# Kernel tuning notes

Measured on AMD Instinct MI355X. Metric: run time of the kernel, lower is better.

The kernel has to match this reference:

```python
import jax, jax.numpy as jnp
import numpy as np


def rosa_batch(bits):
    """Vectorized ROSA (suffix-automaton 'predict next symbol of longest previously
    seen suffix') for a batch of binary sequences.

    bits: [N, T] int32 in {0,1}. Returns [N, T] int32 in {-1, 0, 1}.

    Equivalent to the serial suffix-automaton: at step i, let L = max_{j<i}
    lcs(i, j) (longest common suffix of prefixes ending at i and j). If L == 0
    the answer is -1; otherwise let e = max{ j < i : lcs(i, j) == L } (most
    recent occurrence end, matching the automaton's last-endpos bookkeeping)
    and the answer is bits[e + 1]. lcs follows the standard recurrence
    lcs(i, j) = (x[i] == x[j]) * (lcs(i-1, j-1) + 1), computed with a scan
    over i carrying the length-T lcs row, vmapped implicitly over N.
    """
    N, T = bits.shape
    jpos = jnp.arange(T)

    def step(prev, it):
        i, xt = it  # i: scalar step index, xt: [N] current symbols
        # prev[:, j] = lcs(i-1, j); shift to get lcs(i-1, j-1)
        shifted = jnp.concatenate([jnp.zeros((N, 1), prev.dtype), prev[:, :-1]], axis=1)
        cur = jnp.where(bits == xt[:, None], shifted + 1, 0)  # [N, T] lcs(i, j)
        valid = jpos[None, :] < i
        cm = jnp.where(valid, cur, -1)
        L = cm.max(axis=1)  # [N] longest previously-seen suffix length
        # most recent j < i achieving the max
        e = jnp.where(valid & (cm == L[:, None]), jpos[None, :], -1).max(axis=1)
        nxt = jnp.take_along_axis(bits, jnp.clip(e + 1, 0, T - 1)[:, None], axis=1)[:, 0]
        y = jnp.where(L > 0, nxt, -1)
        return cur, y

    _, ys = jax.lax.scan(step, jnp.zeros((N, T), jnp.int32), (jnp.arange(T), bits.T))
    return ys.T


def rosa_bits_btc(bits_btc):
    """bits_btc: [B, T, C] -> idx [B, T, C]; ROSA runs along T per (b, c)."""
    B, T, C = bits_btc.shape
    seqs = bits_btc.transpose(0, 2, 1).reshape(B * C, T)
    return rosa_batch(seqs).reshape(B, C, T).transpose(0, 2, 1)


def setup_inputs() -> dict:
    key = jax.random.key(0)
    B, T, C = 4, 2048, 128
    x = jax.random.normal(key, (B, T, C), dtype=jnp.float32)
    emb0 = jnp.full((1, 1, C), -1e-5, dtype=jnp.float32)
    emb1 = jnp.full((1, 1, C), 1e-5, dtype=jnp.float32)
    return {"x": x, "emb0": emb0, "emb1": emb1}


def reference(x, emb0, emb1):
    bits = (x > 0).astype(jnp.int32)
    idx = rosa_bits_btc(bits)  # [B, T, C] in {-1, 0, 1}
    return jnp.where(idx == -1, jnp.zeros_like(x), jnp.where(idx == 1, emb1, emb0))
```

## Files before the change

kernel.cpp:

```cpp
#include <hip/hip_runtime.h>


#define TT 2048
#define CC 128
#define NW 64
#define NSEQ 512
#define SBITS_WORDS (NSEQ * NW)
#define RES_WORDS (NSEQ * TT)

typedef short          s16x2 __attribute__((ext_vector_type(2)));
typedef unsigned short u16x2 __attribute__((ext_vector_type(2)));

__device__ __forceinline__ unsigned pk_sign(unsigned x) {
    s16x2 v = __builtin_bit_cast(s16x2, x);
    v = v >> 15;
    return __builtin_bit_cast(unsigned, v);
}
__device__ __forceinline__ unsigned pk_shl1(unsigned x) {
    u16x2 v = __builtin_bit_cast(u16x2, x);
    v = v << 1;
    return __builtin_bit_cast(unsigned, v);
}
__device__ __forceinline__ unsigned pk_add8(unsigned x) {
    u16x2 v = __builtin_bit_cast(u16x2, x);
    v = v + (unsigned short)8;
    return __builtin_bit_cast(unsigned, v);
}
__device__ __forceinline__ unsigned pk_maxu(unsigned a, unsigned b) {
    u16x2 x = __builtin_bit_cast(u16x2, a);
    u16x2 y = __builtin_bit_cast(u16x2, b);
    u16x2 r = __builtin_elementwise_max(x, y);
    return __builtin_bit_cast(unsigned, r);
}

__global__ void k_bits(const float* __restrict__ x, unsigned* __restrict__ sbits)
{
    const int b = blockIdx.x >> 6;
    const int w = blockIdx.x & 63;
    const int t = threadIdx.x;
    __shared__ unsigned char sbyt[32 * 132];

    #pragma unroll
    for (int r = 0; r < 16; ++r) {
        const int e  = t + (r << 8);
        const int ii = e >> 7;
        const int c  = e & 127;
        const float v = x[((size_t)(b * TT + (w << 5) + ii)) * CC + c];
        sbyt[ii * 132 + c] = (v > 0.0f) ? 1u : 0u;
    }
    __syncthreads();

    if (t < CC) {
        unsigned word = 0u;
        #pragma unroll
        for (int ii = 0; ii < 32; ++ii)
            word |= (unsigned)(sbyt[ii * 132 + t] & 1u) << ii;
        sbits[((b << 7) | t) * NW + w] = word;
    }
}

__global__ __launch_bounds__(256, 4) void k_dp2(
    const unsigned* __restrict__ sbits, unsigned* __restrict__ res)
{
    const int u = blockIdx.x;
    const int q = blockIdx.y;
    int k = 0;
    #pragma unroll
    for (int kk = 1; kk < 8; ++kk) if (u >= (kk * (kk + 1)) / 2) k = kk;
    const int chunk = u - (k * (k + 1)) / 2;
    const int D0 = 1 + (chunk << 8);

    const int tid  = threadIdx.x;
    const int lane = tid & 63;
    const int wv   = tid >> 6;
    const int g    = lane >> 3;
    const int lm   = lane & 7;
    const int wB   = k << 3;
    const int wloc = wB + lm;
    const int kb   = k << 8;

    __shared__ unsigned pad[128];
    __shared__ unsigned seedl[256];
    __shared__ unsigned wres[4][8][33];

    if (tid < 64) pad[tid] = 0u;
    else if (tid < 128) pad[tid] = sbits[q * NW + (tid - 64)];
    __syncthreads();

    {
        const int d = D0 + tid;
        unsigned acc = 0u;
        if (d < kb) {
            const int dw = d >> 5, dr = d & 31;
            for (int w = wB - 1; w >= 0; --w) {
                const int sw = w - dw;
                const unsigned u0 = pad[64 + sw];
                const unsigned u1 = pad[63 + sw];
                const unsigned shw = dr ? ((u0 << dr) | (u1 >> (32 - dr))) : u0;
                const unsigned ew = (sw > 0) ? 0xFFFFFFFFu
                                  : ((sw == 0) ? (0xFFFFFFFFu << dr) : 0u);
                const unsigned mw = (~(pad[64 + w] ^ shw)) & ew;
                const unsigned t2 = (mw == 0xFFFFFFFFu) ? 32u
                                  : (unsigned)__builtin_clz(~mw);
                acc += t2;
                if (t2 < 32u) break;
            }
        }
        seedl[tid] = acc;
    }
    __syncthreads();

    const unsigned a = pad[64 + wloc];

    unsigned lmaxp[16];
    #pragma unroll
    for (int j = 0; j < 16; ++j) lmaxp[j] = 0u;

    #pragma unroll
    for (int it = 0; it < 8; ++it) {
        const int d  = D0 + (it << 5) + (wv << 3) + g;
        const int dw = d >> 5;
        const int dr = d & 31;

        const int s = wloc - dw;
        const unsigned b0 = pad[64 + s];
        const unsigned b1 = pad[63 + s];
        const unsigned sh = dr ? ((b0 << dr) | (b1 >> (32 - dr))) : b0;
        const unsigned em = (s > 0) ? 0xFFFFFFFFu
                          : ((s == 0) ? (0xFFFFFFFFu << dr) : 0u);
        const unsigned m = (~(a ^ sh)) & em;

        const unsigned seedv = seedl[(it << 5) + (wv << 3) + g];
        const unsigned pm = (unsigned)__shfl_up((int)m, 1, 64);
        const unsigned lead = (unsigned)__builtin_clz(~pm | 1u);
        unsigned inc = (lm == 0) ? seedv : lead;

        if (__builtin_expect(
                __ballot((lm > 0) && (pm == 0xFFFFFFFFu)) != 0ULL, 0)) {
            if ((lm > 0) && (pm == 0xFFFFFFFFu)) {
                unsigned acc = 0u;
                int w;
                for (w = wloc - 1; w >= wB; --w) {
                    const int sw = w - dw;
                    const unsigned u0 = pad[64 + sw];
                    const unsigned u1 = pad[63 + sw];
                    const unsigned shw = dr ? ((u0 << dr) | (u1 >> (32 - dr))) : u0;
                    const unsigned ew = (sw > 0) ? 0xFFFFFFFFu
                                      : ((sw == 0) ? (0xFFFFFFFFu << dr) : 0u);
                    const unsigned mw = (~(pad[64 + w] ^ shw)) & ew;
                    const unsigned t2 = (mw == 0xFFFFFFFFu) ? 32u
                                      : (unsigned)__builtin_clz(~mw);
                    acc += t2;
                    if (t2 < 32u) break;
                }
                if (w < wB) acc += seedv;
                inc = acc;
            }
        }

        const unsigned nm   = ~m;
        const unsigned u16c = (unsigned)__builtin_clz((nm << 16) | 0x8000u);
        const unsigned s16  = u16c + ((u16c == 16u) ? inc : 0u);

        const unsigned itc  = 7u - (unsigned)it;
        const unsigned itc2 = itc * 0x10001u;
        unsigned rp = ((inc << 3) | itc) | (((s16 << 3) | itc) << 16);

        const unsigned mr  = __builtin_bitreverse32(m);
        unsigned mmr = (mr >> 16) | (mr << 16);

        #pragma unroll
        for (int j = 0; j < 16; ++j) {
            const unsigned sm = pk_sign(mmr);
            mmr = pk_shl1(mmr);
            rp  = pk_add8(rp);
            rp  = (rp & sm) | (itc2 & ~sm);
            lmaxp[j] = pk_maxu(lmaxp[j], rp);
        }
    }

    unsigned lm32[32];
    const unsigned Kp = 2048u - (unsigned)(D0 + (wv << 3) + g) - 224u;
    #pragma unroll
    for (int j = 0; j < 16; ++j) {
        const unsigned v  = lmaxp[j];
        const unsigned lo = v & 0xFFFFu;
        const unsigned hi = v >> 16;
        lm32[j]      = ((lo & 0xFFF8u) << 8) + ((lo & 7u) << 5) + Kp;
        lm32[16 + j] = ((hi & 0xFFF8u) << 8) + ((hi & 7u) << 5) + Kp;
    }

    #pragma unroll
    for (int bb = 0; bb < 32; ++bb) {
        unsigned v = lm32[bb];
        v = max(v, (unsigned)__shfl_xor((int)v, 8, 64));
        v = max(v, (unsigned)__shfl_xor((int)v, 16, 64));
        v = max(v, (unsigned)__shfl_xor((int)v, 32, 64));
        lm32[bb] = v;
    }
    if (lane < 8) {
        #pragma unroll
        for (int bb = 0; bb < 32; ++bb) wres[wv][lane][bb] = lm32[bb];
    }
    __syncthreads();

    {
        const int lw = tid >> 5, bb = tid & 31;
        const unsigned v = max(max(wres[0][lw][bb], wres[1][lw][bb]),
                               max(wres[2][lw][bb], wres[3][lw][bb]));
        if (v >> 11) {
            const int i = ((wB + lw) << 5) + bb;
            atomicMax(&res[(size_t)q * TT + i], v);
        }
    }
}

__global__ void k_dec(const unsigned* __restrict__ sbits,
                      const unsigned* __restrict__ res,
                      const float* __restrict__ emb0,
                      const float* __restrict__ emb1,
                      float* __restrict__ out)
{
    const int b  = blockIdx.y;
    const int i0 = blockIdx.x << 4;
    const int t  = threadIdx.x;
    __shared__ float trans[16][CC + 4];

    const int c  = t >> 1;
    const int q8 = (t & 1) << 3;
    const unsigned* rp = res + ((size_t)((b << 7) | c) * TT) + i0 + q8;
    const unsigned* bw = sbits + ((size_t)((b << 7) | c)) * NW;
    const float e0 = emb0[c], e1 = emb1[c];

    #pragma unroll
    for (int jj = 0; jj < 8; ++jj) {
        const unsigned v = rp[jj];
        const int i = i0 + q8 + jj;
        float val = 0.0f;
        if (v >> 11) {
            const int d   = TT - (int)(v & 2047u);
            const int e1p = i - d + 1;
            val = ((bw[e1p >> 5] >> (e1p & 31)) & 1u) ? e1 : e0;
        }
        trans[q8 + jj][c] = val;
    }
    __syncthreads();

    const int ii = t >> 4;
    const int c0 = (t & 15) << 3;
    float4 w0 = *(const float4*)&trans[ii][c0];
    float4 w1 = *(const float4*)&trans[ii][c0 + 4];
    float* op = out + ((size_t)(b * TT + i0 + ii)) * CC + c0;
    *(float4*)op       = w0;
    *(float4*)(op + 4) = w1;
}

extern "C" void kernel_launch(void* const* d_in, const int* in_sizes, int n_in,
                              void* d_out, int out_size, void* d_ws, size_t ws_size,
                              hipStream_t stream)
{
    const float* x    = (const float*)d_in[0];
    const float* emb0 = (const float*)d_in[1];
    const float* emb1 = (const float*)d_in[2];
    float* out        = (float*)d_out;

    unsigned* sbits = (unsigned*)d_ws;
    unsigned* res   = (unsigned*)d_ws + SBITS_WORDS;

    hipMemsetAsync((void*)res, 0, (size_t)RES_WORDS * 4, stream);
    k_bits<<<dim3(4 * 64), dim3(256), 0, stream>>>(x, sbits);
    k_dp2<<<dim3(36, NSEQ), dim3(256), 0, stream>>>(sbits, res);
    k_dec<<<dim3(TT / 16, 4), dim3(256), 0, stream>>>(sbits, res, emb0, emb1, out);
}
```

Before: 166.0 us.

## Pack lane index into 16-bit keys and reduce packed pairs with a slow overflow fallback

Re-encodes the per-lane max key into 16-bit halves (10-bit saturating length, 3-bit iteration, 3-bit lane), so the cross-lane shuffle reduction runs on 16 packed registers instead of 32 widened words. Each lane then writes only 4 decoded results to shared memory. When any wave sees a saturated length, a slower exact fallback recomputes 32-bit keys from the saved inc values. This cuts shuffle and unpack work in the common case, at the cost of extra registers for incs and a divergent fallback path.

```diff
diff --git a/kernel.cpp b/kernel.cpp
--- a/kernel.cpp
+++ b/kernel.cpp
@@ -21,9 +21,10 @@
     v = v << 1;
     return __builtin_bit_cast(unsigned, v);
 }
-__device__ __forceinline__ unsigned pk_add8(unsigned x) {
+__device__ __forceinline__ unsigned pk_addsat64(unsigned x) {
     u16x2 v = __builtin_bit_cast(u16x2, x);
-    v = v + (unsigned short)8;
+    u16x2 c = {64, 64};
+    v = __builtin_elementwise_add_sat(v, c);
     return __builtin_bit_cast(unsigned, v);
 }
 __device__ __forceinline__ unsigned pk_maxu(unsigned a, unsigned b) {
@@ -115,6 +116,8 @@
     unsigned lmaxp[16];
     #pragma unroll
     for (int j = 0; j < 16; ++j) lmaxp[j] = 0u;
+
+    unsigned incs[8];
 
     #pragma unroll
     for (int it = 0; it < 8; ++it) {
@@ -157,14 +160,16 @@
                 inc = acc;
             }
         }
+        incs[it] = inc;
 
         const unsigned nm   = ~m;
         const unsigned u16c = (unsigned)__builtin_clz((nm << 16) | 0x8000u);
         const unsigned s16  = u16c + ((u16c == 16u) ? inc : 0u);
 
-        const unsigned itc  = 7u - (unsigned)it;
-        const unsigned itc2 = itc * 0x10001u;
-        unsigned rp = ((inc << 3) | itc) | (((s16 << 3) | itc) << 16);
+        const unsigned itcv = (unsigned)((7 - it) << 3) * 0x10001u;
+        const unsigned ci = inc > 1023u ? 1023u : inc;
+        const unsigned cs = s16 > 1023u ? 1023u : s16;
+        unsigned rp = (ci << 6) | (cs << 22) | itcv;
 
         const unsigned mr  = __builtin_bitreverse32(m);
         unsigned mmr = (mr >> 16) | (mr << 16);
@@ -173,34 +178,75 @@
         for (int j = 0; j < 16; ++j) {
             const unsigned sm = pk_sign(mmr);
             mmr = pk_shl1(mmr);
-            rp  = pk_add8(rp);
-            rp  = (rp & sm) | (itc2 & ~sm);
+            rp  = pk_addsat64(rp);
+            rp  = (rp & sm) | (itcv & ~sm);
             lmaxp[j] = pk_maxu(lmaxp[j], rp);
         }
     }
 
-    unsigned lm32[32];
-    const unsigned Kp = 2048u - (unsigned)(D0 + (wv << 3) + g) - 224u;
+    const unsigned gk2 = (unsigned)(7 - g) * 0x10001u;
+    #pragma unroll
+    for (int j = 0; j < 16; ++j) lmaxp[j] |= gk2;
+
     #pragma unroll
     for (int j = 0; j < 16; ++j) {
-        const unsigned v  = lmaxp[j];
-        const unsigned lo = v & 0xFFFFu;
-        const unsigned hi = v >> 16;
-        lm32[j]      = ((lo & 0xFFF8u) << 8) + ((lo & 7u) << 5) + Kp;
-        lm32[16 + j] = ((hi & 0xFFF8u) << 8) + ((hi & 7u) << 5) + Kp;
-    }
-
-    #pragma unroll
-    for (int bb = 0; bb < 32; ++bb) {
-        unsigned v = lm32[bb];
-        v = max(v, (unsigned)__shfl_xor((int)v, 8, 64));
-        v = max(v, (unsigned)__shfl_xor((int)v, 16, 64));
-        v = max(v, (unsigned)__shfl_xor((int)v, 32, 64));
-        lm32[bb] = v;
-    }
-    if (lane < 8) {
-        #pragma unroll
-        for (int bb = 0; bb < 32; ++bb) wres[wv][lane][bb] = lm32[bb];
+        unsigned v = lmaxp[j];
+        v = pk_maxu(v, (unsigned)__shfl_xor((int)v, 8, 64));
+        v = pk_maxu(v, (unsigned)__shfl_xor((int)v, 16, 64));
+        v = pk_maxu(v, (unsigned)__shfl_xor((int)v, 32, 64));
+        lmaxp[j] = v;
+    }
+
+    unsigned mx = lmaxp[0];
+    #pragma unroll
+    for (int j = 1; j < 16; ++j) mx = pk_maxu(mx, lmaxp[j]);
+    const bool ovf = ((mx & 0x0000FC00u) == 0x0000FC00u) ||
+                     ((mx & 0xFC000000u) == 0xFC000000u);
+
+    if (__builtin_expect(__ballot(ovf) == 0ULL, 1)) {
+        const unsigned Kw = 2048u - (unsigned)D0 - (unsigned)(wv << 3) - 231u;
+        #pragma unroll
+        for (int e = 0; e < 4; ++e) {
+            const int j = ((g & 3) << 2) + e;
+            const unsigned r32 = lmaxp[j];
+            const unsigned h = (g >= 4) ? (r32 >> 16) : (r32 & 0xFFFFu);
+            const unsigned v = ((h >> 6) << 11) + ((h & 0x38u) << 2) + (h & 7u) + Kw;
+            wres[wv][lm][(g << 2) + e] = v;
+        }
+    } else {
+        unsigned lm32[32];
+        #pragma unroll
+        for (int bb = 0; bb < 32; ++bb) lm32[bb] = 0u;
+        for (int it = 0; it < 8; ++it) {
+            const int d  = D0 + (it << 5) + (wv << 3) + g;
+            const int dw = d >> 5;
+            const int dr = d & 31;
+            const unsigned dcode = (unsigned)(TT - d) & 2047u;
+            const int s = wloc - dw;
+            const unsigned b0 = pad[64 + s];
+            const unsigned b1 = pad[63 + s];
+            const unsigned sh = dr ? ((b0 << dr) | (b1 >> (32 - dr))) : b0;
+            const unsigned em = (s > 0) ? 0xFFFFFFFFu
+                              : ((s == 0) ? (0xFFFFFFFFu << dr) : 0u);
+            const unsigned m = (~(a ^ sh)) & em;
+            unsigned pkv = (incs[it] << 11) | dcode;
+            for (int bb = 0; bb < 32; ++bb) {
+                pkv = ((m >> bb) & 1u) ? (pkv + 0x800u) : dcode;
+                lm32[bb] = lm32[bb] >= pkv ? lm32[bb] : pkv;
+            }
+        }
+        #pragma unroll
+        for (int bb = 0; bb < 32; ++bb) {
+            unsigned v = lm32[bb];
+            v = max(v, (unsigned)__shfl_xor((int)v, 8, 64));
+            v = max(v, (unsigned)__shfl_xor((int)v, 16, 64));
+            v = max(v, (unsigned)__shfl_xor((int)v, 32, 64));
+            lm32[bb] = v;
+        }
+        if (g == 0) {
+            #pragma unroll
+            for (int bb = 0; bb < 32; ++bb) wres[wv][lm][bb] = lm32[bb];
+        }
     }
     __syncthreads();
 
```

After: 168.9 us. No clear change (+1.7%).
